# Optimization experiments

Measured on AMD Instinct MI355X. Metric: run time of the kernel, lower is better.

The kernel has to match this reference:

```python
import jax, jax.numpy as jnp
import numpy as np

N = 50000
E_RAND = 800000
F_IN = 256
F_OUT = 256
ALPHA = 0.2  # LeakyReLU negative slope


def setup_inputs() -> dict:
    key = jax.random.key(0)
    k1, k2, k3, k4 = jax.random.split(key, 4)
    x = jax.random.normal(k1, (N, F_IN), dtype=jnp.float32)
    # random edges + self-loops so every row has at least one edge (avoids div by 0)
    edge_rand = jax.random.randint(k2, (2, E_RAND), 0, N)
    loops = jnp.arange(N)
    edge = jnp.concatenate([edge_rand, jnp.stack([loops, loops])], axis=1)  # [2, 850000]
    W = jax.random.normal(k3, (F_IN, F_OUT), dtype=jnp.float32) * 0.05
    a = jax.random.normal(k4, (2 * F_OUT,), dtype=jnp.float32) * 0.05
    return {"x": x, "edge": edge, "W": W, "a": a}


def reference(x, edge, W, a):
    # x: [N, F_in], edge: [2, E] (row = dst/aggregation index per torch.sparse.mm(a, h))
    n = x.shape[0]
    f_out = W.shape[1]
    h = x @ W  # [N, F_out]
    src, dst = edge[0], edge[1]
    # a @ [h_src; h_dst] decomposes into two per-node dot products (no [E, 2F] concat)
    s = h @ a[:f_out]   # [N]
    t = h @ a[f_out:]   # [N]
    logit = s[src] + t[dst]                                  # [E]
    e = jnp.exp(-jax.nn.leaky_relu(logit, ALPHA))            # [E]
    rowsum = jax.ops.segment_sum(e, src, num_segments=n)     # [N]
    msg = e[:, None] * h[dst]                                # [E, F_out]
    h_prime = jax.ops.segment_sum(msg, src, num_segments=n)  # [N, F_out]
    h_prime = h_prime / rowsum[:, None]
    return jax.nn.relu(h_prime)  # concat=True path
```

## Files before the change

### kernel.cpp

```cpp
#include <hip/hip_runtime.h>
#include <hip/hip_fp16.h>

#define FDIM 256
#define ALPHA 0.2f

typedef _Float16 half8 __attribute__((ext_vector_type(8)));
typedef float floatx4 __attribute__((ext_vector_type(4)));
typedef float fltx4 __attribute__((ext_vector_type(4)));
typedef int intx2 __attribute__((ext_vector_type(2)));

__global__ __launch_bounds__(256) void prep_w(const float* __restrict__ W,
                                              _Float16* __restrict__ wswz) {
  const int g = blockIdx.x * 256 + threadIdx.x;
  const int kc = g >> 11, L = g & 2047;
  const int n = L >> 3, c = L & 7;
  half8 hv;
#pragma unroll
  for (int j = 0; j < 8; ++j)
    hv[j] = (_Float16)W[(size_t)(kc * 64 + c * 8 + j) * 256 + n];
  *(half8*)(wswz + (size_t)g * 8) = hv;
}

#define HT_STRIDE 264
__global__ __launch_bounds__(256) void gemm_hist(
    const float* __restrict__ x, const _Float16* __restrict__ wswz,
    const float* __restrict__ a, _Float16* __restrict__ h,
    float* __restrict__ s, float* __restrict__ t, int M,
    const int* __restrict__ edge, int* __restrict__ deg, int E, int nblk) {
  if ((int)blockIdx.x >= nblk) {
    const int e = ((int)blockIdx.x - nblk) * 256 + threadIdx.x;
    if (e < E) atomicAdd(&deg[edge[e]], 1);
    return;
  }
  __shared__ __align__(16) _Float16 smem[64 * HT_STRIDE];
  _Float16* As = smem;
  const int tid = threadIdx.x;
  const int w = tid >> 6, l = tid & 63;
  const int l15 = l & 15, q = l >> 4;
  const int row0 = blockIdx.x * 64;

  floatx4 acc[4][4];
#pragma unroll
  for (int mt = 0; mt < 4; ++mt)
#pragma unroll
    for (int nt = 0; nt < 4; ++nt) acc[mt][nt] = (floatx4){0.f, 0.f, 0.f, 0.f};

  const int id0 = tid, id1 = 256 + tid;
  const int m0 = id0 >> 3, c0 = (id0 & 7) ^ (m0 & 7);
  const int m1 = id1 >> 3, c1 = (id1 & 7) ^ (m1 & 7);
  const int r0 = row0 + m0, r1 = row0 + m1;

  float4 pf[2][2];
  auto loadA = [&](int kc) {
    pf[0][0] = pf[0][1] = pf[1][0] = pf[1][1] = make_float4(0.f, 0.f, 0.f, 0.f);
    if (r0 < M) {
      const float4* p = (const float4*)(x + (size_t)r0 * 256 + kc * 64 + c0 * 8);
      pf[0][0] = p[0];
      pf[0][1] = p[1];
    }
    if (r1 < M) {
      const float4* p = (const float4*)(x + (size_t)r1 * 256 + kc * 64 + c1 * 8);
      pf[1][0] = p[0];
      pf[1][1] = p[1];
    }
  };
  auto storeA = [&]() {
#pragma unroll
    for (int hf = 0; hf < 2; ++hf) {
      half8 hv;
      hv[0] = (_Float16)pf[hf][0].x; hv[1] = (_Float16)pf[hf][0].y;
      hv[2] = (_Float16)pf[hf][0].z; hv[3] = (_Float16)pf[hf][0].w;
      hv[4] = (_Float16)pf[hf][1].x; hv[5] = (_Float16)pf[hf][1].y;
      hv[6] = (_Float16)pf[hf][1].z; hv[7] = (_Float16)pf[hf][1].w;
      *(half8*)(As + (size_t)(hf * 256 + tid) * 8) = hv;
    }
  };

  loadA(0);
  for (int kc = 0; kc < 4; ++kc) {
    storeA();
    half8 bf[2][4];
#pragma unroll
    for (int ks = 0; ks < 2; ++ks) {
      const int c = ks * 4 + q;
#pragma unroll
      for (int nt = 0; nt < 4; ++nt) {
        const int n = w * 64 + nt * 16 + l15;
        bf[ks][nt] = *(const half8*)(wswz + (size_t)(kc * 2048 + n * 8 + c) * 8);
      }
    }
    __syncthreads();
    if (kc < 3) loadA(kc + 1);
#pragma unroll
    for (int ks = 0; ks < 2; ++ks) {
      const int c = ks * 4 + q;
      half8 af[4];
#pragma unroll
      for (int mt = 0; mt < 4; ++mt) {
        const int m = mt * 16 + l15;
        af[mt] = *(const half8*)(As + (size_t)(m * 8 + (c ^ (m & 7))) * 8);
      }
#pragma unroll
      for (int mt = 0; mt < 4; ++mt)
#pragma unroll
        for (int nt = 0; nt < 4; ++nt)
          acc[mt][nt] = __builtin_amdgcn_mfma_f32_16x16x32_f16(
              af[mt], bf[ks][nt], acc[mt][nt], 0, 0, 0);
    }
    __syncthreads();
  }

#pragma unroll
  for (int mt = 0; mt < 4; ++mt)
#pragma unroll
    for (int nt = 0; nt < 4; ++nt)
#pragma unroll
      for (int r = 0; r < 4; ++r)
        smem[(size_t)(mt * 16 + q * 4 + r) * HT_STRIDE + w * 64 + nt * 16 +
             l15] = (_Float16)acc[mt][nt][r];
  __syncthreads();

  const int w8 = tid >> 5;
  const int colh = (tid & 31) * 8;
#pragma unroll
  for (int p = 0; p < 8; ++p) {
    const int rl = p * 8 + w8;
    const int row = row0 + rl;
    if (row < M)
      *(half8*)(h + (size_t)row * 256 + colh) =
          *(const half8*)(smem + (size_t)rl * HT_STRIDE + colh);
  }

  const int r8 = tid >> 2, seg = tid & 3;
  float sp = 0.f, tp = 0.f;
#pragma unroll
  for (int c8 = 0; c8 < 8; ++c8) {
    const int col = seg * 64 + c8 * 8;
    const half8 hv = *(const half8*)(smem + (size_t)r8 * HT_STRIDE + col);
    const float4 a0 = *(const float4*)(a + col);
    const float4 a1 = *(const float4*)(a + col + 4);
    const float4 b0 = *(const float4*)(a + 256 + col);
    const float4 b1 = *(const float4*)(a + 256 + col + 4);
    sp += (float)hv[0] * a0.x + (float)hv[1] * a0.y + (float)hv[2] * a0.z +
          (float)hv[3] * a0.w + (float)hv[4] * a1.x + (float)hv[5] * a1.y +
          (float)hv[6] * a1.z + (float)hv[7] * a1.w;
    tp += (float)hv[0] * b0.x + (float)hv[1] * b0.y + (float)hv[2] * b0.z +
          (float)hv[3] * b0.w + (float)hv[4] * b1.x + (float)hv[5] * b1.y +
          (float)hv[6] * b1.z + (float)hv[7] * b1.w;
  }
  sp += __shfl_xor(sp, 1);
  sp += __shfl_xor(sp, 2);
  tp += __shfl_xor(tp, 1);
  tp += __shfl_xor(tp, 2);
  if (seg == 0 && row0 + r8 < M) {
    s[row0 + r8] = sp;
    t[row0 + r8] = tp;
  }
}

__global__ __launch_bounds__(1024) void scan1(const int* __restrict__ deg,
                                              int* __restrict__ rowstart,
                                              int* __restrict__ bsum, int n) {
  const int tid = threadIdx.x;
  const int i = blockIdx.x * 1024 + tid;
  const int val = (i < n) ? deg[i] : 0;
  const int lane = tid & 63, wv = tid >> 6;
  int v = val;
#pragma unroll
  for (int off = 1; off < 64; off <<= 1) {
    const int o = __shfl_up(v, off);
    if (lane >= off) v += o;
  }
  __shared__ int wsum[16];
  __shared__ int woff[16];
  if (lane == 63) wsum[wv] = v;
  __syncthreads();
  if (tid < 16) {
    int wv2 = wsum[tid];
#pragma unroll
    for (int off = 1; off < 16; off <<= 1) {
      const int o = __shfl_up(wv2, off);
      if (tid >= off) wv2 += o;
    }
    woff[tid] = wv2;
  }
  __syncthreads();
  const int incl = v + (wv ? woff[wv - 1] : 0);
  if (i < n) rowstart[i] = incl - val;
  if (tid == 1023) bsum[blockIdx.x] = woff[15];
}

__global__ __launch_bounds__(1024) void scan23(const int* __restrict__ bsum,
                                               int* __restrict__ rowstart,
                                               int* __restrict__ rsc, int nb,
                                               int n) {
  __shared__ int boffsh[64];
  const int tid = threadIdx.x;
  if (tid < 64) {
    int v = (tid < nb) ? bsum[tid] : 0;
#pragma unroll
    for (int off = 1; off < 64; off <<= 1) {
      const int o = __shfl_up(v, off);
      if (tid >= off) v += o;
    }
    boffsh[tid] = v;
    if (tid == nb - 1) rowstart[n] = v;
  }
  __syncthreads();
  for (int i = tid; i < n; i += 1024) {
    const int b = i >> 10;
    const int v = rowstart[i] + (b ? boffsh[b - 1] : 0);
    rowstart[i] = v;
    rsc[i] = v;
  }
}

__global__ void scatter_kernel(const int* __restrict__ edge,
                               int* __restrict__ rsc,
                               const float* __restrict__ s,
                               const float* __restrict__ t,
                               int2* __restrict__ sde, int E) {
  const int e = blockIdx.x * 256 + threadIdx.x;
  if (e < E) {
    const int src = edge[e];
    const int dst = edge[E + e];
    const float logit = s[src] + t[dst];
    const float lr = logit > 0.f ? logit : ALPHA * logit;
    const float ev = __expf(-lr);
    const int pos = atomicAdd(&rsc[src], 1);
    sde[pos] = make_int2(dst, __float_as_int(ev));
  }
}

__global__ __launch_bounds__(256) void agg_kernel(
    const _Float16* __restrict__ h, const int* __restrict__ rowstart,
    const int2* __restrict__ sde, float* __restrict__ out, int n) {
  const int w = threadIdx.x >> 6, l = threadIdx.x & 63;
  const int row = blockIdx.x * 4 + w;
  if (row >= n) return;
  const int start = rowstart[row], end = rowstart[row + 1];
  const int half = l >> 5;
  const int lh = l & 31;
  const size_t fo = (size_t)lh * 8;
  float acc[8] = {};
  float rs = 0.f;
  int j = start;
  for (; j + 8 <= end; j += 8) {
#pragma unroll
    for (int u = 0; u < 4; ++u) {
      const int2 p = sde[j + u * 2 + half];
      const half8 v = *(const half8*)(h + (size_t)p.x * 256 + fo);
      const float e = __int_as_float(p.y);
      rs += e;
#pragma unroll
      for (int k = 0; k < 8; ++k) acc[k] += e * (float)v[k];
    }
  }
  for (; j < end; j += 2) {
    const int idx = j + half;
    const bool valid = idx < end;
    const int2 p = valid ? sde[idx] : make_int2(0, 0);
    const half8 v = *(const half8*)(h + (size_t)p.x * 256 + fo);
    const float e = valid ? __int_as_float(p.y) : 0.f;
    rs += e;
#pragma unroll
    for (int k = 0; k < 8; ++k) acc[k] += e * (float)v[k];
  }
  rs += __shfl_xor(rs, 32);
#pragma unroll
  for (int k = 0; k < 8; ++k) acc[k] += __shfl_xor(acc[k], 32);
  const float inv = 1.f / rs;
  float4 o;
#pragma unroll
  for (int k = 0; k < 4; ++k) {
    const float vv = acc[half * 4 + k] * inv;
    (&o.x)[k] = vv > 0.f ? vv : 0.f;
  }
  *(float4*)(out + (size_t)row * 256 + lh * 8 + half * 4) = o;
}

extern "C" void kernel_launch(void* const* d_in, const int* in_sizes, int n_in,
                              void* d_out, int out_size, void* d_ws,
                              size_t ws_size, hipStream_t stream) {
  const float* x = (const float*)d_in[0];
  const int* edge = (const int*)d_in[1];
  const float* W = (const float*)d_in[2];
  const float* a = (const float*)d_in[3];
  float* out = (float*)d_out;
  const int N = in_sizes[0] / FDIM;
  const int E = in_sizes[1] / 2;
  const int NB = (N + 1023) / 1024;
  const int NBLK_GEMM = (N + 63) / 64;
  const int NBLK_HIST = (E + 255) / 256;

  _Float16* h = (_Float16*)d_ws;
  _Float16* wswz = h + (size_t)N * FDIM;
  float* s = (float*)(wswz + 8192 * 8);
  float* t = s + N;
  int* deg = (int*)(t + N);
  int* rsc = deg + N;
  int* rowstart = rsc + N;
  int* bsum = rowstart + N + 2;
  int2* sde = (int2*)(bsum + 64);

  hipMemsetAsync(deg, 0, (size_t)N * sizeof(int), stream);

  prep_w<<<32, 256, 0, stream>>>(W, wswz);
  gemm_hist<<<NBLK_GEMM + NBLK_HIST, 256, 0, stream>>>(
      x, wswz, a, h, s, t, N, edge, deg, E, NBLK_GEMM);
  scan1<<<NB, 1024, 0, stream>>>(deg, rowstart, bsum, N);
  scan23<<<1, 1024, 0, stream>>>(bsum, rowstart, rsc, NB, N);
  scatter_kernel<<<(E + 255) / 256, 256, 0, stream>>>(edge, rsc, s, t, sde, E);
  agg_kernel<<<(N + 3) / 4, 256, 0, stream>>>(h, rowstart, sde, out, N);
}
```

Baseline: 271.1 us.

## Split GEMM blocks across output halves and replace serial scan fixup with per-block offsets

The GEMM is split so each block computes half of the 256 output columns. This doubles the block count, lowers accumulator register use (launch bounds now request 5 blocks per SIMD) and halves the LDS staging stride. Partial s/t dot products are combined with float atomics into zero-initialised buffers. The single-block scan23 pass, which rewrote all rowstart entries serially, is replaced by a tiny 64-thread block-offset scan. The scatter and aggregation kernels then add the per-1024-row block offset on the fly. The trade-off is extra atomics and duplicated A-tile loads and conversions per row block.

Result: faster. 260.5 us (-3.9%).

```diff
diff --git a/kernel.cpp b/kernel.cpp
--- a/kernel.cpp
+++ b/kernel.cpp
@@ -6,7 +6,6 @@
 
 typedef _Float16 half8 __attribute__((ext_vector_type(8)));
 typedef float floatx4 __attribute__((ext_vector_type(4)));
-typedef float fltx4 __attribute__((ext_vector_type(4)));
 typedef int intx2 __attribute__((ext_vector_type(2)));
 
 __global__ __launch_bounds__(256) void prep_w(const float* __restrict__ W,
@@ -21,8 +20,8 @@
   *(half8*)(wswz + (size_t)g * 8) = hv;
 }
 
-#define HT_STRIDE 264
-__global__ __launch_bounds__(256) void gemm_hist(
+#define HT_STRIDE 132
+__global__ __launch_bounds__(256, 5) void gemm_hist(
     const float* __restrict__ x, const _Float16* __restrict__ wswz,
     const float* __restrict__ a, _Float16* __restrict__ h,
     float* __restrict__ s, float* __restrict__ t, int M,
@@ -37,13 +36,14 @@
   const int tid = threadIdx.x;
   const int w = tid >> 6, l = tid & 63;
   const int l15 = l & 15, q = l >> 4;
-  const int row0 = blockIdx.x * 64;
-
-  floatx4 acc[4][4];
+  const int nh = blockIdx.x & 1;
+  const int row0 = (blockIdx.x >> 1) * 64;
+
+  floatx4 acc[4][2];
 #pragma unroll
   for (int mt = 0; mt < 4; ++mt)
 #pragma unroll
-    for (int nt = 0; nt < 4; ++nt) acc[mt][nt] = (floatx4){0.f, 0.f, 0.f, 0.f};
+    for (int nt = 0; nt < 2; ++nt) acc[mt][nt] = (floatx4){0.f, 0.f, 0.f, 0.f};
 
   const int id0 = tid, id1 = 256 + tid;
   const int m0 = id0 >> 3, c0 = (id0 & 7) ^ (m0 & 7);
@@ -79,13 +79,13 @@
   loadA(0);
   for (int kc = 0; kc < 4; ++kc) {
     storeA();
-    half8 bf[2][4];
+    half8 bf[2][2];
 #pragma unroll
     for (int ks = 0; ks < 2; ++ks) {
       const int c = ks * 4 + q;
 #pragma unroll
-      for (int nt = 0; nt < 4; ++nt) {
-        const int n = w * 64 + nt * 16 + l15;
+      for (int nt = 0; nt < 2; ++nt) {
+        const int n = nh * 128 + w * 32 + nt * 16 + l15;
         bf[ks][nt] = *(const half8*)(wswz + (size_t)(kc * 2048 + n * 8 + c) * 8);
       }
     }
@@ -103,7 +103,7 @@
 #pragma unroll
       for (int mt = 0; mt < 4; ++mt)
 #pragma unroll
-        for (int nt = 0; nt < 4; ++nt)
+        for (int nt = 0; nt < 2; ++nt)
           acc[mt][nt] = __builtin_amdgcn_mfma_f32_16x16x32_f16(
               af[mt], bf[ks][nt], acc[mt][nt], 0, 0, 0);
     }
@@ -113,34 +113,35 @@
 #pragma unroll
   for (int mt = 0; mt < 4; ++mt)
 #pragma unroll
-    for (int nt = 0; nt < 4; ++nt)
+    for (int nt = 0; nt < 2; ++nt)
 #pragma unroll
       for (int r = 0; r < 4; ++r)
-        smem[(size_t)(mt * 16 + q * 4 + r) * HT_STRIDE + w * 64 + nt * 16 +
+        smem[(size_t)(mt * 16 + q * 4 + r) * HT_STRIDE + w * 32 + nt * 16 +
              l15] = (_Float16)acc[mt][nt][r];
   __syncthreads();
 
-  const int w8 = tid >> 5;
-  const int colh = (tid & 31) * 8;
-#pragma unroll
-  for (int p = 0; p < 8; ++p) {
-    const int rl = p * 8 + w8;
+  const int w16 = tid >> 4;
+  const int colh = (tid & 15) * 8;
+#pragma unroll
+  for (int p = 0; p < 4; ++p) {
+    const int rl = p * 16 + w16;
     const int row = row0 + rl;
     if (row < M)
-      *(half8*)(h + (size_t)row * 256 + colh) =
+      *(half8*)(h + (size_t)row * 256 + nh * 128 + colh) =
           *(const half8*)(smem + (size_t)rl * HT_STRIDE + colh);
   }
 
   const int r8 = tid >> 2, seg = tid & 3;
   float sp = 0.f, tp = 0.f;
 #pragma unroll
-  for (int c8 = 0; c8 < 8; ++c8) {
-    const int col = seg * 64 + c8 * 8;
+  for (int c8 = 0; c8 < 4; ++c8) {
+    const int col = seg * 32 + c8 * 8;
+    const int acol = nh * 128 + col;
     const half8 hv = *(const half8*)(smem + (size_t)r8 * HT_STRIDE + col);
-    const float4 a0 = *(const float4*)(a + col);
-    const float4 a1 = *(const float4*)(a + col + 4);
-    const float4 b0 = *(const float4*)(a + 256 + col);
-    const float4 b1 = *(const float4*)(a + 256 + col + 4);
+    const float4 a0 = *(const float4*)(a + acol);
+    const float4 a1 = *(const float4*)(a + acol + 4);
+    const float4 b0 = *(const float4*)(a + 256 + acol);
+    const float4 b1 = *(const float4*)(a + 256 + acol + 4);
     sp += (float)hv[0] * a0.x + (float)hv[1] * a0.y + (float)hv[2] * a0.z +
           (float)hv[3] * a0.w + (float)hv[4] * a1.x + (float)hv[5] * a1.y +
           (float)hv[6] * a1.z + (float)hv[7] * a1.w;
@@ -153,13 +154,14 @@
   tp += __shfl_xor(tp, 1);
   tp += __shfl_xor(tp, 2);
   if (seg == 0 && row0 + r8 < M) {
-    s[row0 + r8] = sp;
-    t[row0 + r8] = tp;
+    atomicAdd(&s[row0 + r8], sp);
+    atomicAdd(&t[row0 + r8], tp);
   }
 }
 
 __global__ __launch_bounds__(1024) void scan1(const int* __restrict__ deg,
                                               int* __restrict__ rowstart,
+                                              int* __restrict__ rsc,
                                               int* __restrict__ bsum, int n) {
   const int tid = threadIdx.x;
   const int i = blockIdx.x * 1024 + tid;
@@ -186,40 +188,32 @@
   }
   __syncthreads();
   const int incl = v + (wv ? woff[wv - 1] : 0);
-  if (i < n) rowstart[i] = incl - val;
+  if (i < n) {
+    const int ex = incl - val;
+    rowstart[i] = ex;
+    rsc[i] = ex;
+    if (i == n - 1) rowstart[n] = incl;
+  }
   if (tid == 1023) bsum[blockIdx.x] = woff[15];
 }
 
-__global__ __launch_bounds__(1024) void scan23(const int* __restrict__ bsum,
-                                               int* __restrict__ rowstart,
-                                               int* __restrict__ rsc, int nb,
-                                               int n) {
-  __shared__ int boffsh[64];
+__global__ __launch_bounds__(64) void scan2(const int* __restrict__ bsum,
+                                            int* __restrict__ boffx, int nb) {
   const int tid = threadIdx.x;
-  if (tid < 64) {
-    int v = (tid < nb) ? bsum[tid] : 0;
-#pragma unroll
-    for (int off = 1; off < 64; off <<= 1) {
-      const int o = __shfl_up(v, off);
-      if (tid >= off) v += o;
-    }
-    boffsh[tid] = v;
-    if (tid == nb - 1) rowstart[n] = v;
-  }
-  __syncthreads();
-  for (int i = tid; i < n; i += 1024) {
-    const int b = i >> 10;
-    const int v = rowstart[i] + (b ? boffsh[b - 1] : 0);
-    rowstart[i] = v;
-    rsc[i] = v;
-  }
-}
-
-__global__ void scatter_kernel(const int* __restrict__ edge,
-                               int* __restrict__ rsc,
-                               const float* __restrict__ s,
-                               const float* __restrict__ t,
-                               int2* __restrict__ sde, int E) {
+  const int bval = (tid < nb) ? bsum[tid] : 0;
+  int v = bval;
+#pragma unroll
+  for (int off = 1; off < 64; off <<= 1) {
+    const int o = __shfl_up(v, off);
+    if (tid >= off) v += o;
+  }
+  if (tid < nb) boffx[tid] = v - bval;
+}
+
+__global__ __launch_bounds__(256) void scatter_kernel(
+    const int* __restrict__ edge, int* __restrict__ rsc,
+    const int* __restrict__ boffx, const float* __restrict__ s,
+    const float* __restrict__ t, int2* __restrict__ sde, int E) {
   const int e = blockIdx.x * 256 + threadIdx.x;
   if (e < E) {
     const int src = edge[e];
@@ -227,18 +221,20 @@
     const float logit = s[src] + t[dst];
     const float lr = logit > 0.f ? logit : ALPHA * logit;
     const float ev = __expf(-lr);
-    const int pos = atomicAdd(&rsc[src], 1);
+    const int pos = atomicAdd(&rsc[src], 1) + boffx[src >> 10];
     sde[pos] = make_int2(dst, __float_as_int(ev));
   }
 }
 
 __global__ __launch_bounds__(256) void agg_kernel(
     const _Float16* __restrict__ h, const int* __restrict__ rowstart,
-    const int2* __restrict__ sde, float* __restrict__ out, int n) {
+    const int* __restrict__ boffx, const int2* __restrict__ sde,
+    float* __restrict__ out, int n) {
   const int w = threadIdx.x >> 6, l = threadIdx.x & 63;
   const int row = blockIdx.x * 4 + w;
   if (row >= n) return;
-  const int start = rowstart[row], end = rowstart[row + 1];
+  const int start = rowstart[row] + boffx[row >> 10];
+  const int end = rowstart[row + 1] + boffx[(row + 1) >> 10];
   const int half = l >> 5;
   const int lh = l & 31;
   const size_t fo = (size_t)lh * 8;
@@ -290,7 +286,7 @@
   const int N = in_sizes[0] / FDIM;
   const int E = in_sizes[1] / 2;
   const int NB = (N + 1023) / 1024;
-  const int NBLK_GEMM = (N + 63) / 64;
+  const int NBLK_GEMM = ((N + 63) / 64) * 2;
   const int NBLK_HIST = (E + 255) / 256;
 
   _Float16* h = (_Float16*)d_ws;
@@ -301,15 +297,17 @@
   int* rsc = deg + N;
   int* rowstart = rsc + N;
   int* bsum = rowstart + N + 2;
-  int2* sde = (int2*)(bsum + 64);
-
-  hipMemsetAsync(deg, 0, (size_t)N * sizeof(int), stream);
+  int* boffx = bsum + 64;
+  int2* sde = (int2*)(boffx + 64);
+
+  hipMemsetAsync(s, 0, (size_t)N * 3 * sizeof(int), stream);
 
   prep_w<<<32, 256, 0, stream>>>(W, wswz);
   gemm_hist<<<NBLK_GEMM + NBLK_HIST, 256, 0, stream>>>(
       x, wswz, a, h, s, t, N, edge, deg, E, NBLK_GEMM);
-  scan1<<<NB, 1024, 0, stream>>>(deg, rowstart, bsum, N);
-  scan23<<<1, 1024, 0, stream>>>(bsum, rowstart, rsc, NB, N);
-  scatter_kernel<<<(E + 255) / 256, 256, 0, stream>>>(edge, rsc, s, t, sde, E);
-  agg_kernel<<<(N + 3) / 4, 256, 0, stream>>>(h, rowstart, sde, out, N);
-}
+  scan1<<<NB, 1024, 0, stream>>>(deg, rowstart, rsc, bsum, N);
+  scan2<<<1, 64, 0, stream>>>(bsum, boffx, NB);
+  scatter_kernel<<<(E + 255) / 256, 256, 0, stream>>>(edge, rsc, boffx, s, t,
+                                                      sde, E);
+  agg_kernel<<<(N + 3) / 4, 256, 0, stream>>>(h, rowstart, boffx, sde, out, N);
+}
```
